# Kernel tuning notes

Hardware: AMD Instinct MI355X
Metric: run time of the kernel (lower is better)

The kernel has to match this reference:

```python
import jax, jax.numpy as jnp
import numpy as np
from jax.ops import segment_sum, segment_max

N = 100000
E = 1600000
IN_C, HID, OUT_C, HEADS = 4, 64, 1, 2
HC = HID // HEADS  # 32 per-head channels


def setup_inputs() -> dict:
    key = jax.random.key(0)
    ks = jax.random.split(key, 12)
    s = lambda fan_in: 1.0 / np.sqrt(fan_in)
    x = jax.random.normal(ks[0], (N, IN_C), dtype=jnp.float32)
    edge_index = jax.random.randint(ks[1], (2, E), 0, N, dtype=jnp.int32)
    return {
        "x": x,
        "edge_index": edge_index,
        "gcn1_w": jax.random.uniform(ks[2], (IN_C, HID), jnp.float32, -s(IN_C), s(IN_C)),
        "gcn1_b": jnp.zeros((HID,), jnp.float32),
        "gat_wl": jax.random.uniform(ks[3], (HID, HID), jnp.float32, -s(HID), s(HID)),
        "gat_wr": jax.random.uniform(ks[4], (HID, HID), jnp.float32, -s(HID), s(HID)),
        "gat_att": jax.random.uniform(ks[5], (HEADS, HC), jnp.float32, -s(HC), s(HC)),
        "gat_b": jnp.zeros((HID,), jnp.float32),
        "gcn2_w": jax.random.uniform(ks[6], (HID, HID), jnp.float32, -s(HID), s(HID)),
        "gcn2_b": jnp.zeros((HID,), jnp.float32),
        "out_w": jax.random.uniform(ks[7], (HID, OUT_C), jnp.float32, -s(HID), s(HID)),
        "out_b": jnp.zeros((OUT_C,), jnp.float32),
    }


def _add_self_loops(edge_index):
    loop = jnp.arange(N, dtype=edge_index.dtype)
    src = jnp.concatenate([edge_index[0], loop])
    dst = jnp.concatenate([edge_index[1], loop])
    return src, dst


def _gcn(x, src, dst, W, b):
    # x' = D^{-1/2} (A+I) D^{-1/2} x W + b  (self-loops already in src/dst)
    h = x @ W  # [N, F]
    deg = segment_sum(jnp.ones_like(dst, dtype=h.dtype), dst, num_segments=N)
    dinv = jnp.where(deg > 0, jax.lax.rsqrt(jnp.maximum(deg, 1e-12)), 0.0)
    norm = dinv[src] * dinv[dst]  # [E']
    out = segment_sum(h[src] * norm[:, None], dst, num_segments=N)
    return out + b


def _gatv2(x, src, dst, Wl, Wr, att, b):
    # GATv2: e_ij = a^T LeakyReLU(Wl x_j + Wr x_i); softmax over in-neighbors of i
    hl = (x @ Wl).reshape(N, HEADS, HC)  # source transform
    hr = (x @ Wr).reshape(N, HEADS, HC)  # target transform
    e = jax.nn.leaky_relu(hl[src] + hr[dst], negative_slope=0.2)  # [E', H, C]
    logits = jnp.einsum("ehc,hc->eh", e, att)  # [E', H]
    m = segment_max(logits, dst, num_segments=N)  # [N, H]
    m = jnp.where(jnp.isfinite(m), m, 0.0)
    ex = jnp.exp(logits - m[dst])
    denom = segment_sum(ex, dst, num_segments=N)  # [N, H]
    alpha = ex / (denom[dst] + 1e-16)  # [E', H]  (dropout skipped: eval mode)
    out = segment_sum(alpha[:, :, None] * hl[src], dst, num_segments=N)  # [N, H, C]
    return out.reshape(N, HEADS * HC) + b


def reference(x, edge_index, gcn1_w, gcn1_b, gat_wl, gat_wr, gat_att, gat_b,
              gcn2_w, gcn2_b, out_w, out_b):
    src, dst = _add_self_loops(edge_index)
    h = jax.nn.relu(_gcn(x, src, dst, gcn1_w, gcn1_b))
    h = jax.nn.relu(_gatv2(h, src, dst, gat_wl, gat_wr, gat_att, gat_b))
    h = jax.nn.relu(_gcn(h, src, dst, gcn2_w, gcn2_b))
    return h @ out_w + out_b
```

## Files before the change

### kernel.cpp

```cpp
#include <hip/hip_runtime.h>
#include <hip/hip_fp16.h>
#include <math.h>

#define N_NODES 100000
#define N_EDGES 1600000
#define HID 64
#define NB 391
#define CAP 4608
#define SCAP (CAP + 256)

__device__ __forceinline__ float leaky02(float v) { return (v > 0.f) ? v : 0.2f * v; }

__device__ __forceinline__ void unpack_h8(uint4 u, float* v) {
    float2 f0 = __half22float2(*(__half2*)&u.x);
    float2 f1 = __half22float2(*(__half2*)&u.y);
    float2 f2 = __half22float2(*(__half2*)&u.z);
    float2 f3 = __half22float2(*(__half2*)&u.w);
    v[0] = f0.x; v[1] = f0.y; v[2] = f1.x; v[3] = f1.y;
    v[4] = f2.x; v[5] = f2.y; v[6] = f3.x; v[7] = f3.y;
}
__device__ __forceinline__ uint4 pack_h8(const float* v) {
    __half2 a = __floats2half2_rn(v[0], v[1]);
    __half2 b = __floats2half2_rn(v[2], v[3]);
    __half2 c = __floats2half2_rn(v[4], v[5]);
    __half2 d = __floats2half2_rn(v[6], v[7]);
    uint4 u;
    u.x = *(unsigned int*)&a; u.y = *(unsigned int*)&b;
    u.z = *(unsigned int*)&c; u.w = *(unsigned int*)&d;
    return u;
}

__global__ void k_bin_scatter(const int* __restrict__ src, const int* __restrict__ dst,
                              int* __restrict__ gcur, unsigned int* __restrict__ binned) {
    __shared__ int hist[NB];
    __shared__ int base[NB];
    for (int t = threadIdx.x; t < NB; t += blockDim.x) hist[t] = 0;
    __syncthreads();
    int stride = gridDim.x * blockDim.x;
    int gid = blockIdx.x * blockDim.x + threadIdx.x;
    for (int e = gid; e < N_EDGES; e += stride)
        atomicAdd(&hist[dst[e] >> 8], 1);
    __syncthreads();
    for (int t = threadIdx.x; t < NB; t += blockDim.x) {
        int h = hist[t];
        base[t] = h ? atomicAdd(&gcur[t], h) : 0;
        hist[t] = 0;
    }
    __syncthreads();
    for (int e = gid; e < N_EDGES; e += stride) {
        int d = dst[e];
        int bkt = d >> 8;
        int off = base[bkt] + atomicAdd(&hist[bkt], 1);
        binned[(size_t)bkt * CAP + off] = (unsigned int)src[e] | ((unsigned int)(d & 255) << 24);
    }
}

__global__ void __launch_bounds__(256) k_node_scan(
        const unsigned int* __restrict__ binned, const int* __restrict__ gcur,
        const float* __restrict__ x, int* __restrict__ rowbeg, int* __restrict__ rowend,
        float* __restrict__ dinv, float* __restrict__ xs, int* __restrict__ srcs) {
    __shared__ unsigned int stash[CAP];
    __shared__ int c[256];
    __shared__ int scan[256];
    int b = blockIdx.x, t = threadIdx.x;
    int n0 = b << 8;
    int ne = gcur[b];
    c[t] = 1;
    __syncthreads();
    for (int i = t; i < ne; i += 256) {
        unsigned int v = binned[(size_t)b * CAP + i];
        stash[i] = v;
        atomicAdd(&c[v >> 24], 1);
    }
    __syncthreads();
    int cnt = c[t];
    scan[t] = cnt;
    __syncthreads();
    for (int off = 1; off < 256; off <<= 1) {
        int add = (t >= off) ? scan[t - off] : 0;
        __syncthreads();
        scan[t] += add;
        __syncthreads();
    }
    int rb = b * SCAP + (scan[t] - cnt);
    int gn = n0 + t;
    if (gn < N_NODES) {
        rowbeg[gn] = rb;
        rowend[gn] = rb + cnt;
        float di = rsqrtf((float)cnt);
        dinv[gn] = di;
        float4 xv = ((const float4*)x)[gn];
        xv.x *= di; xv.y *= di; xv.z *= di; xv.w *= di;
        ((float4*)xs)[gn] = xv;
    }
    __syncthreads();
    c[t] = rb;
    __syncthreads();
    for (int i = t; i < ne; i += 256) {
        unsigned int v = stash[i];
        int pos = atomicAdd(&c[v >> 24], 1);
        srcs[pos] = (int)(v & 0xFFFFFFu);
    }
    __syncthreads();
    if (gn < N_NODES) srcs[c[t]] = gn;
}

__global__ void __launch_bounds__(256) k_aggx_hlhr(
        const int* __restrict__ rowbeg, const int* __restrict__ rowend,
        const int* __restrict__ srcs, const float* __restrict__ xs,
        const float* __restrict__ dinv, const float* __restrict__ W1,
        const float* __restrict__ b1, const float* __restrict__ Wl,
        const float* __restrict__ Wr, __half* __restrict__ hl,
        float* __restrict__ hr) {
    __shared__ float4 aggx_t[32];
    __shared__ float h1[32 * HID];
    int lane = threadIdx.x & 63;
    int w    = threadIdx.x >> 6;
    int g    = threadIdx.x >> 4;
    int q    = threadIdx.x & 15;
    int n0   = blockIdx.x * 32;
#pragma unroll
    for (int k = 0; k < 2; ++k) {
        int n = g * 2 + k;
        int i = n0 + n;
        int rb = rowbeg[i], re = rowend[i];
        float4 acc = {0.f, 0.f, 0.f, 0.f};
        for (int p = rb + q; p < re; p += 16) {
            float4 v = ((const float4*)xs)[srcs[p]];
            acc.x += v.x; acc.y += v.y; acc.z += v.z; acc.w += v.w;
        }
#pragma unroll
        for (int mask = 1; mask <= 8; mask <<= 1) {
            acc.x += __shfl_xor(acc.x, mask);
            acc.y += __shfl_xor(acc.y, mask);
            acc.z += __shfl_xor(acc.z, mask);
            acc.w += __shfl_xor(acc.w, mask);
        }
        if (q == 0) {
            float di = dinv[i];
            acc.x *= di; acc.y *= di; acc.z *= di; acc.w *= di;
            aggx_t[n] = acc;
        }
    }
    __syncthreads();
    float w10 = W1[0 * HID + lane], w11 = W1[1 * HID + lane];
    float w12 = W1[2 * HID + lane], w13 = W1[3 * HID + lane];
    float bb  = b1[lane];
#pragma unroll
    for (int j = 0; j < 8; ++j) {
        int n = w * 8 + j;
        float4 a = aggx_t[n];
        h1[n * HID + lane] = fmaxf(a.x * w10 + a.y * w11 + a.z * w12 + a.w * w13 + bb, 0.f);
    }
    __syncthreads();
    float al[8], ar[8];
#pragma unroll
    for (int j = 0; j < 8; ++j) { al[j] = 0.f; ar[j] = 0.f; }
#pragma unroll 2
    for (int k0 = 0; k0 < 16; ++k0) {
        float wl0 = Wl[(k0 * 4 + 0) * HID + lane];
        float wl1 = Wl[(k0 * 4 + 1) * HID + lane];
        float wl2 = Wl[(k0 * 4 + 2) * HID + lane];
        float wl3 = Wl[(k0 * 4 + 3) * HID + lane];
        float wr0 = Wr[(k0 * 4 + 0) * HID + lane];
        float wr1 = Wr[(k0 * 4 + 1) * HID + lane];
        float wr2 = Wr[(k0 * 4 + 2) * HID + lane];
        float wr3 = Wr[(k0 * 4 + 3) * HID + lane];
#pragma unroll
        for (int j = 0; j < 8; ++j) {
            const float4 hv = *(const float4*)(&h1[(w * 8 + j) * HID + k0 * 4]);
            al[j] += hv.x * wl0 + hv.y * wl1 + hv.z * wl2 + hv.w * wl3;
            ar[j] += hv.x * wr0 + hv.y * wr1 + hv.z * wr2 + hv.w * wr3;
        }
    }
#pragma unroll
    for (int j = 0; j < 8; ++j) {
        int gn = n0 + w * 8 + j;
        hl[(size_t)gn * HID + lane] = __float2half(al[j]);
        hr[(size_t)gn * HID + lane] = ar[j];
    }
}

__global__ void __launch_bounds__(256) k_gat(
        const int* __restrict__ rowbeg, const int* __restrict__ rowend,
        const int* __restrict__ srcs,
        const __half* __restrict__ hl, const float* __restrict__ hr,
        const float* __restrict__ att, const float* __restrict__ gat_b,
        const float* __restrict__ dinv, __half* __restrict__ s2) {
    int lane = threadIdx.x & 63;
    int w    = threadIdx.x >> 6;
    int h    = lane >> 5;
    int g    = (lane & 31) >> 3;
    int q    = lane & 7;
    int c0   = q * 8;
    int i    = blockIdx.x * 8 + w * 2 + h;
    float hri[8], a8[8];
    {
        const float4 t0 = *(const float4*)(hr + (size_t)i * HID + c0);
        const float4 t1 = *(const float4*)(hr + (size_t)i * HID + c0 + 4);
        hri[0] = t0.x; hri[1] = t0.y; hri[2] = t0.z; hri[3] = t0.w;
        hri[4] = t1.x; hri[5] = t1.y; hri[6] = t1.z; hri[7] = t1.w;
        const float4 u0 = *(const float4*)(att + c0);
        const float4 u1 = *(const float4*)(att + c0 + 4);
        a8[0] = u0.x; a8[1] = u0.y; a8[2] = u0.z; a8[3] = u0.w;
        a8[4] = u1.x; a8[5] = u1.y; a8[6] = u1.z; a8[7] = u1.w;
    }
    float m = -1e30f, denom = 0.f;
    float acc[8];
#pragma unroll
    for (int j = 0; j < 8; ++j) acc[j] = 0.f;
    int b = rowbeg[i], en = rowend[i];
    int p = b + g;
    for (; p + 4 < en; p += 8) {
        int s0 = srcs[p];
        int s1 = srcs[p + 4];
        float v0[8], v1[8];
        unpack_h8(*(const uint4*)(hl + (size_t)s0 * HID + c0), v0);
        unpack_h8(*(const uint4*)(hl + (size_t)s1 * HID + c0), v1);
        float t0 = 0.f, t1 = 0.f;
#pragma unroll
        for (int j = 0; j < 8; ++j) {
            t0 += leaky02(v0[j] + hri[j]) * a8[j];
            t1 += leaky02(v1[j] + hri[j]) * a8[j];
        }
        t0 += __shfl_xor(t0, 1); t1 += __shfl_xor(t1, 1);
        t0 += __shfl_xor(t0, 2); t1 += __shfl_xor(t1, 2);
        float nm = fmaxf(m, t0);
        float sc = __expf(m - nm);
        float ex = __expf(t0 - nm);
        denom = denom * sc + ex;
#pragma unroll
        for (int j = 0; j < 8; ++j) acc[j] = acc[j] * sc + ex * v0[j];
        m = nm;
        nm = fmaxf(m, t1);
        sc = __expf(m - nm);
        ex = __expf(t1 - nm);
        denom = denom * sc + ex;
#pragma unroll
        for (int j = 0; j < 8; ++j) acc[j] = acc[j] * sc + ex * v1[j];
        m = nm;
    }
    if (p < en) {
        int s = srcs[p];
        float v0[8];
        unpack_h8(*(const uint4*)(hl + (size_t)s * HID + c0), v0);
        float t0 = 0.f;
#pragma unroll
        for (int j = 0; j < 8; ++j) t0 += leaky02(v0[j] + hri[j]) * a8[j];
        t0 += __shfl_xor(t0, 1);
        t0 += __shfl_xor(t0, 2);
        float nm = fmaxf(m, t0);
        float sc = __expf(m - nm);
        float ex = __expf(t0 - nm);
        denom = denom * sc + ex;
#pragma unroll
        for (int j = 0; j < 8; ++j) acc[j] = acc[j] * sc + ex * v0[j];
        m = nm;
    }
#pragma unroll
    for (int mask = 8; mask <= 16; mask <<= 1) {
        float m2 = __shfl_xor(m, mask);
        float d2 = __shfl_xor(denom, mask);
        float a2[8];
#pragma unroll
        for (int j = 0; j < 8; ++j) a2[j] = __shfl_xor(acc[j], mask);
        float nm = fmaxf(m, m2);
        float sa = __expf(m - nm);
        float sb = __expf(m2 - nm);
        denom = denom * sa + d2 * sb;
#pragma unroll
        for (int j = 0; j < 8; ++j) acc[j] = acc[j] * sa + a2[j] * sb;
        m = nm;
    }
    float inv = 1.f / (denom + 1e-16f);
    float gb8[8];
    {
        const float4 u0 = *(const float4*)(gat_b + c0);
        const float4 u1 = *(const float4*)(gat_b + c0 + 4);
        gb8[0] = u0.x; gb8[1] = u0.y; gb8[2] = u0.z; gb8[3] = u0.w;
        gb8[4] = u1.x; gb8[5] = u1.y; gb8[6] = u1.z; gb8[7] = u1.w;
    }
    float di = dinv[i];
    float o[8];
#pragma unroll
    for (int j = 0; j < 8; ++j) o[j] = fmaxf(acc[j] * inv + gb8[j], 0.f) * di;
    if (g == 0) *(uint4*)(s2 + (size_t)i * HID + c0) = pack_h8(o);
}

__global__ void __launch_bounds__(256) k_agg2_out(
        const int* __restrict__ rowbeg, const int* __restrict__ rowend,
        const int* __restrict__ srcs,
        const __half* __restrict__ s2, const float* __restrict__ dinv,
        const float* __restrict__ W2, const float* __restrict__ b2,
        const float* __restrict__ out_w, const float* __restrict__ out_b,
        float* __restrict__ out) {
    __shared__ float lds[8][HID];
    int lane = threadIdx.x & 63;
    int w    = threadIdx.x >> 6;
    int h    = lane >> 5;
    int g    = (lane & 31) >> 3;
    int q    = lane & 7;
    int c0   = q * 8;
    int i    = blockIdx.x * 8 + w * 2 + h;
    int b = rowbeg[i], en = rowend[i];
    float acc[8];
#pragma unroll
    for (int j = 0; j < 8; ++j) acc[j] = 0.f;
    int p = b + g;
    for (; p + 4 < en; p += 8) {
        int s0 = srcs[p];
        int s1 = srcs[p + 4];
        float v0[8], v1[8];
        unpack_h8(*(const uint4*)(s2 + (size_t)s0 * HID + c0), v0);
        unpack_h8(*(const uint4*)(s2 + (size_t)s1 * HID + c0), v1);
#pragma unroll
        for (int j = 0; j < 8; ++j) acc[j] += v0[j] + v1[j];
    }
    if (p < en) {
        int s = srcs[p];
        float v0[8];
        unpack_h8(*(const uint4*)(s2 + (size_t)s * HID + c0), v0);
#pragma unroll
        for (int j = 0; j < 8; ++j) acc[j] += v0[j];
    }
#pragma unroll
    for (int mask = 8; mask <= 16; mask <<= 1) {
#pragma unroll
        for (int j = 0; j < 8; ++j) acc[j] += __shfl_xor(acc[j], mask);
    }
    if (g == 0) {
        float di = dinv[i];
        int n = w * 2 + h;
        *(float4*)(&lds[n][c0])     = make_float4(acc[0] * di, acc[1] * di, acc[2] * di, acc[3] * di);
        *(float4*)(&lds[n][c0 + 4]) = make_float4(acc[4] * di, acc[5] * di, acc[6] * di, acc[7] * di);
    }
    __syncthreads();
    const float4* r0 = (const float4*)lds[w * 2];
    const float4* r1 = (const float4*)lds[w * 2 + 1];
    float z0 = 0.f, z1 = 0.f;
#pragma unroll 4
    for (int k0 = 0; k0 < 16; ++k0) {
        float w20 = W2[(k0 * 4 + 0) * HID + lane];
        float w21 = W2[(k0 * 4 + 1) * HID + lane];
        float w22 = W2[(k0 * 4 + 2) * HID + lane];
        float w23 = W2[(k0 * 4 + 3) * HID + lane];
        float4 h0 = r0[k0];
        float4 h1 = r1[k0];
        z0 += h0.x * w20 + h0.y * w21 + h0.z * w22 + h0.w * w23;
        z1 += h1.x * w20 + h1.y * w21 + h1.z * w22 + h1.w * w23;
    }
    float bb = b2[lane];
    z0 = fmaxf(z0 + bb, 0.f);
    z1 = fmaxf(z1 + bb, 0.f);
    float ww = out_w[lane];
    float y0 = z0 * ww, y1 = z1 * ww;
#pragma unroll
    for (int mask = 32; mask >= 1; mask >>= 1) {
        y0 += __shfl_xor(y0, mask);
        y1 += __shfl_xor(y1, mask);
    }
    if (lane == 0) {
        int nb = blockIdx.x * 8 + w * 2;
        float ob0 = out_b[0];
        out[nb]     = y0 + ob0;
        out[nb + 1] = y1 + ob0;
    }
}


extern "C" void kernel_launch(void* const* d_in, const int* in_sizes, int n_in,
                              void* d_out, int out_size, void* d_ws, size_t ws_size,
                              hipStream_t stream) {
    const float* x   = (const float*)d_in[0];
    const int*   ei  = (const int*)d_in[1];
    const int*   src = ei;
    const int*   dst = ei + N_EDGES;
    const float* W1  = (const float*)d_in[2];
    const float* b1  = (const float*)d_in[3];
    const float* Wl  = (const float*)d_in[4];
    const float* Wr  = (const float*)d_in[5];
    const float* att = (const float*)d_in[6];
    const float* gb  = (const float*)d_in[7];
    const float* W2  = (const float*)d_in[8];
    const float* b2  = (const float*)d_in[9];
    const float* ow  = (const float*)d_in[10];
    const float* ob  = (const float*)d_in[11];
    float* out = (float*)d_out;

    char* ws = (char*)d_ws;
    size_t o = 0;
    auto alloc = [&](size_t bytes) { size_t r = o; o = (o + bytes + 255) & ~(size_t)255; return r; };
    int*          gcur   = (int*)         (ws + alloc((size_t)NB * 4));
    unsigned int* binned = (unsigned int*)(ws + alloc((size_t)NB * CAP * 4));
    int*          srcs   = (int*)         (ws + alloc((size_t)NB * SCAP * 4));
    int*          rowbeg = (int*)         (ws + alloc((size_t)N_NODES * 4));
    int*          rowend = (int*)         (ws + alloc((size_t)N_NODES * 4));
    float*        dinv   = (float*)       (ws + alloc((size_t)N_NODES * 4));
    float*        xs     = (float*)       (ws + alloc((size_t)N_NODES * 4 * 4));
    __half*       hl     = (__half*)      (ws + alloc((size_t)N_NODES * HID * 2));
    float*        hr     = (float*)       (ws + alloc((size_t)N_NODES * HID * 4));
    __half*       s2     = (__half*)      (ws + alloc((size_t)N_NODES * HID * 2));
    (void)ws_size; (void)n_in; (void)in_sizes; (void)out_size;

    const int nbG   = N_NODES / 32;
    const int nbW2  = N_NODES / 8;

    hipMemsetAsync(gcur, 0, (size_t)NB * 4, stream);
    k_bin_scatter<<<128, 1024, 0, stream>>>(src, dst, gcur, binned);
    k_node_scan<<<NB, 256, 0, stream>>>(binned, gcur, x, rowbeg, rowend, dinv, xs, srcs);
    k_aggx_hlhr<<<nbG, 256, 0, stream>>>(rowbeg, rowend, srcs, xs, dinv, W1, b1, Wl, Wr, hl, hr);
    k_gat<<<nbW2, 256, 0, stream>>>(rowbeg, rowend, srcs, hl, hr, att, gb, dinv, s2);
    k_agg2_out<<<nbW2, 256, 0, stream>>>(rowbeg, rowend, srcs, s2, dinv, W2, b2, ow, ob, out);
}
```

Measured before the change: 208.3 us.

## Drop online-softmax max tracking, use packed fp16 leaky-relu and half hr

Removes the running max and rescaling from the GAT softmax. Exponentials are computed directly with exp2 and attention weights pre-scaled by log2(e), and the cross-lane merge becomes plain sums. The add and LeakyReLU are done with packed fp16 instructions, and the target transform hr is stored in half precision to halve its memory traffic. The change also doubles the bin_scatter grid and folds the dinv scaling into the per-edge accumulation in the final aggregation. This risks overflow if logits grow large and loses some precision in the fp16 activation path.

```diff
diff --git a/kernel.cpp b/kernel.cpp
--- a/kernel.cpp
+++ b/kernel.cpp
@@ -8,17 +8,31 @@
 #define NB 391
 #define CAP 4608
 #define SCAP (CAP + 256)
-
-__device__ __forceinline__ float leaky02(float v) { return (v > 0.f) ? v : 0.2f * v; }
-
-__device__ __forceinline__ void unpack_h8(uint4 u, float* v) {
-    float2 f0 = __half22float2(*(__half2*)&u.x);
-    float2 f1 = __half22float2(*(__half2*)&u.y);
-    float2 f2 = __half22float2(*(__half2*)&u.z);
-    float2 f3 = __half22float2(*(__half2*)&u.w);
-    v[0] = f0.x; v[1] = f0.y; v[2] = f1.x; v[3] = f1.y;
-    v[4] = f2.x; v[5] = f2.y; v[6] = f3.x; v[7] = f3.y;
-}
+#define L2E 1.4426950408889634f
+
+__device__ __forceinline__ unsigned int pk_add(unsigned int a, unsigned int b) {
+    unsigned int r;
+    asm("v_pk_add_f16 %0, %1, %2" : "=v"(r) : "v"(a), "v"(b));
+    return r;
+}
+__device__ __forceinline__ unsigned int pk_min0(unsigned int a) {
+    unsigned int r;
+    asm("v_pk_min_f16 %0, %1, %2" : "=v"(r) : "v"(a), "v"(0u));
+    return r;
+}
+__device__ __forceinline__ unsigned int pk_max0(unsigned int a) {
+    unsigned int r;
+    asm("v_pk_max_f16 %0, %1, %2" : "=v"(r) : "v"(a), "v"(0u));
+    return r;
+}
+__device__ __forceinline__ unsigned int pk_fma(unsigned int a, unsigned int b, unsigned int c) {
+    unsigned int r;
+    asm("v_pk_fma_f16 %0, %1, %2, %3" : "=v"(r) : "v"(a), "v"(b), "v"(c));
+    return r;
+}
+__device__ __forceinline__ float h2lo(unsigned int u) { return __half2float(*(const __half*)&u); }
+__device__ __forceinline__ float h2hi(unsigned int u) { unsigned short s = (unsigned short)(u >> 16); return __half2float(*(const __half*)&s); }
+
 __device__ __forceinline__ uint4 pack_h8(const float* v) {
     __half2 a = __floats2half2_rn(v[0], v[1]);
     __half2 b = __floats2half2_rn(v[2], v[3]);
@@ -111,7 +125,7 @@
         const float* __restrict__ dinv, const float* __restrict__ W1,
         const float* __restrict__ b1, const float* __restrict__ Wl,
         const float* __restrict__ Wr, __half* __restrict__ hl,
-        float* __restrict__ hr) {
+        __half* __restrict__ hrh) {
     __shared__ float4 aggx_t[32];
     __shared__ float h1[32 * HID];
     int lane = threadIdx.x & 63;
@@ -176,15 +190,15 @@
 #pragma unroll
     for (int j = 0; j < 8; ++j) {
         int gn = n0 + w * 8 + j;
-        hl[(size_t)gn * HID + lane] = __float2half(al[j]);
-        hr[(size_t)gn * HID + lane] = ar[j];
+        hl[(size_t)gn * HID + lane]  = __float2half(al[j]);
+        hrh[(size_t)gn * HID + lane] = __float2half(ar[j]);
     }
 }
 
 __global__ void __launch_bounds__(256) k_gat(
         const int* __restrict__ rowbeg, const int* __restrict__ rowend,
         const int* __restrict__ srcs,
-        const __half* __restrict__ hl, const float* __restrict__ hr,
+        const __half* __restrict__ hl, const __half* __restrict__ hrh,
         const float* __restrict__ att, const float* __restrict__ gat_b,
         const float* __restrict__ dinv, __half* __restrict__ s2) {
     int lane = threadIdx.x & 63;
@@ -194,18 +208,18 @@
     int q    = lane & 7;
     int c0   = q * 8;
     int i    = blockIdx.x * 8 + w * 2 + h;
-    float hri[8], a8[8];
+    unsigned int hri[4];
+    float a8[8];
     {
-        const float4 t0 = *(const float4*)(hr + (size_t)i * HID + c0);
-        const float4 t1 = *(const float4*)(hr + (size_t)i * HID + c0 + 4);
-        hri[0] = t0.x; hri[1] = t0.y; hri[2] = t0.z; hri[3] = t0.w;
-        hri[4] = t1.x; hri[5] = t1.y; hri[6] = t1.z; hri[7] = t1.w;
+        uint4 uh = *(const uint4*)(hrh + (size_t)i * HID + c0);
+        hri[0] = uh.x; hri[1] = uh.y; hri[2] = uh.z; hri[3] = uh.w;
         const float4 u0 = *(const float4*)(att + c0);
         const float4 u1 = *(const float4*)(att + c0 + 4);
-        a8[0] = u0.x; a8[1] = u0.y; a8[2] = u0.z; a8[3] = u0.w;
-        a8[4] = u1.x; a8[5] = u1.y; a8[6] = u1.z; a8[7] = u1.w;
-    }
-    float m = -1e30f, denom = 0.f;
+        a8[0] = u0.x * L2E; a8[1] = u0.y * L2E; a8[2] = u0.z * L2E; a8[3] = u0.w * L2E;
+        a8[4] = u1.x * L2E; a8[5] = u1.y * L2E; a8[6] = u1.z * L2E; a8[7] = u1.w * L2E;
+    }
+    const unsigned int c02 = 0x32663266u;
+    float denom = 0.f;
     float acc[8];
 #pragma unroll
     for (int j = 0; j < 8; ++j) acc[j] = 0.f;
@@ -214,63 +228,62 @@
     for (; p + 4 < en; p += 8) {
         int s0 = srcs[p];
         int s1 = srcs[p + 4];
-        float v0[8], v1[8];
-        unpack_h8(*(const uint4*)(hl + (size_t)s0 * HID + c0), v0);
-        unpack_h8(*(const uint4*)(hl + (size_t)s1 * HID + c0), v1);
+        uint4 u0 = *(const uint4*)(hl + (size_t)s0 * HID + c0);
+        uint4 u1 = *(const uint4*)(hl + (size_t)s1 * HID + c0);
+        const unsigned int* p0 = (const unsigned int*)&u0;
+        const unsigned int* p1 = (const unsigned int*)&u1;
         float t0 = 0.f, t1 = 0.f;
 #pragma unroll
-        for (int j = 0; j < 8; ++j) {
-            t0 += leaky02(v0[j] + hri[j]) * a8[j];
-            t1 += leaky02(v1[j] + hri[j]) * a8[j];
+        for (int k = 0; k < 4; ++k) {
+            unsigned int e0 = pk_add(p0[k], hri[k]);
+            unsigned int l0 = pk_fma(pk_min0(e0), c02, pk_max0(e0));
+            t0 = fmaf(h2lo(l0), a8[2 * k], t0);
+            t0 = fmaf(h2hi(l0), a8[2 * k + 1], t0);
+            unsigned int e1 = pk_add(p1[k], hri[k]);
+            unsigned int l1 = pk_fma(pk_min0(e1), c02, pk_max0(e1));
+            t1 = fmaf(h2lo(l1), a8[2 * k], t1);
+            t1 = fmaf(h2hi(l1), a8[2 * k + 1], t1);
         }
         t0 += __shfl_xor(t0, 1); t1 += __shfl_xor(t1, 1);
         t0 += __shfl_xor(t0, 2); t1 += __shfl_xor(t1, 2);
-        float nm = fmaxf(m, t0);
-        float sc = __expf(m - nm);
-        float ex = __expf(t0 - nm);
-        denom = denom * sc + ex;
-#pragma unroll
-        for (int j = 0; j < 8; ++j) acc[j] = acc[j] * sc + ex * v0[j];
-        m = nm;
-        nm = fmaxf(m, t1);
-        sc = __expf(m - nm);
-        ex = __expf(t1 - nm);
-        denom = denom * sc + ex;
-#pragma unroll
-        for (int j = 0; j < 8; ++j) acc[j] = acc[j] * sc + ex * v1[j];
-        m = nm;
+        float ex0 = exp2f(t0);
+        float ex1 = exp2f(t1);
+        denom += ex0 + ex1;
+#pragma unroll
+        for (int k = 0; k < 4; ++k) {
+            acc[2 * k]     = fmaf(h2lo(p0[k]), ex0, acc[2 * k]);
+            acc[2 * k + 1] = fmaf(h2hi(p0[k]), ex0, acc[2 * k + 1]);
+            acc[2 * k]     = fmaf(h2lo(p1[k]), ex1, acc[2 * k]);
+            acc[2 * k + 1] = fmaf(h2hi(p1[k]), ex1, acc[2 * k + 1]);
+        }
     }
     if (p < en) {
         int s = srcs[p];
-        float v0[8];
-        unpack_h8(*(const uint4*)(hl + (size_t)s * HID + c0), v0);
+        uint4 u0 = *(const uint4*)(hl + (size_t)s * HID + c0);
+        const unsigned int* p0 = (const unsigned int*)&u0;
         float t0 = 0.f;
 #pragma unroll
-        for (int j = 0; j < 8; ++j) t0 += leaky02(v0[j] + hri[j]) * a8[j];
+        for (int k = 0; k < 4; ++k) {
+            unsigned int e0 = pk_add(p0[k], hri[k]);
+            unsigned int l0 = pk_fma(pk_min0(e0), c02, pk_max0(e0));
+            t0 = fmaf(h2lo(l0), a8[2 * k], t0);
+            t0 = fmaf(h2hi(l0), a8[2 * k + 1], t0);
+        }
         t0 += __shfl_xor(t0, 1);
         t0 += __shfl_xor(t0, 2);
-        float nm = fmaxf(m, t0);
-        float sc = __expf(m - nm);
-        float ex = __expf(t0 - nm);
-        denom = denom * sc + ex;
-#pragma unroll
-        for (int j = 0; j < 8; ++j) acc[j] = acc[j] * sc + ex * v0[j];
-        m = nm;
+        float ex0 = exp2f(t0);
+        denom += ex0;
+#pragma unroll
+        for (int k = 0; k < 4; ++k) {
+            acc[2 * k]     = fmaf(h2lo(p0[k]), ex0, acc[2 * k]);
+            acc[2 * k + 1] = fmaf(h2hi(p0[k]), ex0, acc[2 * k + 1]);
+        }
     }
 #pragma unroll
     for (int mask = 8; mask <= 16; mask <<= 1) {
-        float m2 = __shfl_xor(m, mask);
-        float d2 = __shfl_xor(denom, mask);
-        float a2[8];
-#pragma unroll
-        for (int j = 0; j < 8; ++j) a2[j] = __shfl_xor(acc[j], mask);
-        float nm = fmaxf(m, m2);
-        float sa = __expf(m - nm);
-        float sb = __expf(m2 - nm);
-        denom = denom * sa + d2 * sb;
-#pragma unroll
-        for (int j = 0; j < 8; ++j) acc[j] = acc[j] * sa + a2[j] * sb;
-        m = nm;
+        denom += __shfl_xor(denom, mask);
+#pragma unroll
+        for (int j = 0; j < 8; ++j) acc[j] += __shfl_xor(acc[j], mask);
     }
     float inv = 1.f / (denom + 1e-16f);
     float gb8[8];
@@ -302,6 +315,7 @@
     int q    = lane & 7;
     int c0   = q * 8;
     int i    = blockIdx.x * 8 + w * 2 + h;
+    float di = dinv[i];
     int b = rowbeg[i], en = rowend[i];
     float acc[8];
 #pragma unroll
@@ -310,18 +324,27 @@
     for (; p + 4 < en; p += 8) {
         int s0 = srcs[p];
         int s1 = srcs[p + 4];
-        float v0[8], v1[8];
-        unpack_h8(*(const uint4*)(s2 + (size_t)s0 * HID + c0), v0);
-        unpack_h8(*(const uint4*)(s2 + (size_t)s1 * HID + c0), v1);
-#pragma unroll
-        for (int j = 0; j < 8; ++j) acc[j] += v0[j] + v1[j];
+        uint4 u0 = *(const uint4*)(s2 + (size_t)s0 * HID + c0);
+        uint4 u1 = *(const uint4*)(s2 + (size_t)s1 * HID + c0);
+        const unsigned int* p0 = (const unsigned int*)&u0;
+        const unsigned int* p1 = (const unsigned int*)&u1;
+#pragma unroll
+        for (int k = 0; k < 4; ++k) {
+            acc[2 * k]     = fmaf(h2lo(p0[k]), di, acc[2 * k]);
+            acc[2 * k + 1] = fmaf(h2hi(p0[k]), di, acc[2 * k + 1]);
+            acc[2 * k]     = fmaf(h2lo(p1[k]), di, acc[2 * k]);
+            acc[2 * k + 1] = fmaf(h2hi(p1[k]), di, acc[2 * k + 1]);
+        }
     }
     if (p < en) {
         int s = srcs[p];
-        float v0[8];
-        unpack_h8(*(const uint4*)(s2 + (size_t)s * HID + c0), v0);
-#pragma unroll
-        for (int j = 0; j < 8; ++j) acc[j] += v0[j];
+        uint4 u0 = *(const uint4*)(s2 + (size_t)s * HID + c0);
+        const unsigned int* p0 = (const unsigned int*)&u0;
+#pragma unroll
+        for (int k = 0; k < 4; ++k) {
+            acc[2 * k]     = fmaf(h2lo(p0[k]), di, acc[2 * k]);
+            acc[2 * k + 1] = fmaf(h2hi(p0[k]), di, acc[2 * k + 1]);
+        }
     }
 #pragma unroll
     for (int mask = 8; mask <= 16; mask <<= 1) {
@@ -329,10 +352,9 @@
         for (int j = 0; j < 8; ++j) acc[j] += __shfl_xor(acc[j], mask);
     }
     if (g == 0) {
-        float di = dinv[i];
         int n = w * 2 + h;
-        *(float4*)(&lds[n][c0])     = make_float4(acc[0] * di, acc[1] * di, acc[2] * di, acc[3] * di);
-        *(float4*)(&lds[n][c0 + 4]) = make_float4(acc[4] * di, acc[5] * di, acc[6] * di, acc[7] * di);
+        *(float4*)(&lds[n][c0])     = make_float4(acc[0], acc[1], acc[2], acc[3]);
+        *(float4*)(&lds[n][c0 + 4]) = make_float4(acc[4], acc[5], acc[6], acc[7]);
     }
     __syncthreads();
     const float4* r0 = (const float4*)lds[w * 2];
@@ -398,17 +420,17 @@
     float*        dinv   = (float*)       (ws + alloc((size_t)N_NODES * 4));
     float*        xs     = (float*)       (ws + alloc((size_t)N_NODES * 4 * 4));
     __half*       hl     = (__half*)      (ws + alloc((size_t)N_NODES * HID * 2));
-    float*        hr     = (float*)       (ws + alloc((size_t)N_NODES * HID * 4));
+    __half*       hrh    = (__half*)      (ws + alloc((size_t)N_NODES * HID * 2));
     __half*       s2     = (__half*)      (ws + alloc((size_t)N_NODES * HID * 2));
     (void)ws_size; (void)n_in; (void)in_sizes; (void)out_size;
 
     const int nbG   = N_NODES / 32;
     const int nbW2  = N_NODES / 8;
 
-    hipMemsetAsync(gcur, 0, (size_t)NB * 4, stream);
-    k_bin_scatter<<<128, 1024, 0, stream>>>(src, dst, gcur, binned);
+    (void)hipMemsetAsync(gcur, 0, (size_t)NB * 4, stream);
+    k_bin_scatter<<<256, 1024, 0, stream>>>(src, dst, gcur, binned);
     k_node_scan<<<NB, 256, 0, stream>>>(binned, gcur, x, rowbeg, rowend, dinv, xs, srcs);
-    k_aggx_hlhr<<<nbG, 256, 0, stream>>>(rowbeg, rowend, srcs, xs, dinv, W1, b1, Wl, Wr, hl, hr);
-    k_gat<<<nbW2, 256, 0, stream>>>(rowbeg, rowend, srcs, hl, hr, att, gb, dinv, s2);
+    k_aggx_hlhr<<<nbG, 256, 0, stream>>>(rowbeg, rowend, srcs, xs, dinv, W1, b1, Wl, Wr, hl, hrh);
+    k_gat<<<nbW2, 256, 0, stream>>>(rowbeg, rowend, srcs, hl, hrh, att, gb, dinv, s2);
     k_agg2_out<<<nbW2, 256, 0, stream>>>(rowbeg, rowend, srcs, s2, dinv, W2, b2, ow, ob, out);
 }
```

Result: faster. 191.8 us, median of 2 (-7.9%).
